# Kernel tuning notes

Hardware: AMD Instinct MI355X
Metric: run time of the kernel (lower is better)

The kernel has to match this reference:

```python
import jax, jax.numpy as jnp
import numpy as np

B, S = 16, 1024
D_MODEL, N_MEL = 256, 80
IN_DIM = D_MODEL * (((N_MEL - 1) // 2 - 1) // 2)  # 4864
G, V, CV_DIM = 2, 320, 256


def setup_inputs() -> dict:
    key = jax.random.key(0)
    k1, k2, k3 = jax.random.split(key, 3)
    hidden_states = jax.random.normal(k1, (B, S, IN_DIM), dtype=jnp.float32)
    W = jax.random.normal(k2, (IN_DIM, G * V), dtype=jnp.float32) / np.sqrt(IN_DIM)
    b = jnp.zeros((G * V,), dtype=jnp.float32)
    codevectors = jax.random.normal(k3, (1, G * V, CV_DIM // G), dtype=jnp.float32)
    return {"hidden_states": hidden_states, "W": W, "b": b,
            "codevectors": codevectors, "num_groups": G}


def reference(hidden_states, W, b, codevectors, num_groups):
    bsz, seq, _ = hidden_states.shape
    logits = hidden_states @ W + b                      # (B, S, G*V)
    gv = logits.shape[-1]
    nvars = gv // num_groups
    flat = logits.reshape(bsz * seq, num_groups, nvars)  # (BS, G, V)
    idx = jnp.argmax(flat, axis=-1)                      # (BS, G) int
    # one-hot codevector probs (eval / hard argmax branch)
    probs = jax.nn.one_hot(idx, nvars, dtype=logits.dtype)  # (BS, G, V)
    marginal = probs.mean(axis=0)                        # (G, V)
    perplexity = jnp.exp(-jnp.sum(marginal * jnp.log(marginal + 1e-7), axis=-1)).sum()
    # weighted sum over codebook == gather of selected codevector per group
    cv = codevectors.reshape(num_groups, nvars, -1)      # (G, V, Dg)
    gathered = cv[jnp.arange(num_groups)[None, :], idx]  # (BS, G, Dg)
    out = gathered.reshape(bsz, seq, -1)                 # (B, S, codevector_dim)
    return (out, perplexity)
```

## Files before the change

kernel.cpp:

```cpp
#include <hip/hip_runtime.h>
#include <stdint.h>

#define M_TOT 16384
#define K_TOT 4864
#define N_TOT 640
#define GRP   2
#define NV    320
#define CVD   128

#define BM 128
#define BN 320
#define BK 32
#define KITERS (K_TOT / BK)

#define MARGIN 2.0e-3f

typedef __attribute__((ext_vector_type(8))) short short8;
typedef __attribute__((ext_vector_type(4))) float f32x4;

#define WS_FLAGCNT  0
#define WS_COUNTS   256
#define WS_FLAGLIST 4096
#define WS_PACKED   (4096 + 262144)
#define WS_WT       (1u << 20)

__device__ __forceinline__ unsigned int mono_u32(float f) {
    unsigned int b = __float_as_uint(f);
    return b ^ ((unsigned int)((int)b >> 31) | 0x80000000u);
}
__device__ __forceinline__ unsigned short f2bf(float x) {
    unsigned int u = __float_as_uint(x);
    return (unsigned short)((u + 0x7fffu + ((u >> 16) & 1u)) >> 16);
}
__device__ __forceinline__ float bf2f(unsigned short h) {
    return __uint_as_float(((unsigned int)h) << 16);
}
__device__ __forceinline__ void gld16(const void* g, void* l) {
    __builtin_amdgcn_global_load_lds(
        (const __attribute__((address_space(1))) unsigned int*)g,
        (__attribute__((address_space(3))) unsigned int*)l, 16, 0, 0);
}

__global__ __launch_bounds__(256)
void convert_wt(const float* __restrict__ W, unsigned short* __restrict__ wt)
{
    __shared__ float sW[64][68];
    const int k0 = blockIdx.x * 64;
    const int n0 = blockIdx.y * 64;
    const int tid = threadIdx.x;
    for (int l = tid; l < 64 * 16; l += 256) {
        int kr = l >> 4, nc = (l & 15) * 4;
        float4 v = *(const float4*)(W + (size_t)(k0 + kr) * N_TOT + n0 + nc);
        sW[kr][nc] = v.x; sW[kr][nc + 1] = v.y; sW[kr][nc + 2] = v.z; sW[kr][nc + 3] = v.w;
    }
    __syncthreads();
    unsigned short* whi = wt;
    unsigned short* wlo = wt + (size_t)N_TOT * K_TOT;
    for (int l = tid; l < 64 * 8; l += 256) {
        int nr = l >> 3, ko = (l & 7) * 8;
        union { short8 v; unsigned short u[8]; } hu, lu;
#pragma unroll
        for (int j = 0; j < 8; ++j) {
            float x = sW[ko + j][nr];
            unsigned short hb = f2bf(x);
            hu.u[j] = hb;
            lu.u[j] = f2bf(x - bf2f(hb));
        }
        size_t off = (size_t)(n0 + nr) * K_TOT + k0 + ko;
        *(short8*)(whi + off) = hu.v;
        *(short8*)(wlo + off) = lu.v;
    }
}

__device__ __forceinline__ void stage_b(const unsigned short* __restrict__ wt,
                                        short* sBbuf, int bx, int kk, int tid)
{
#pragma unroll
    for (int r = 0; r < 5; ++r) {
        int c = r * 512 + tid;
        int half = (c >= 1280) ? 1 : 0;
        int cc = c - half * 1280;
        int row = cc >> 2, oct = cc & 3;
        const unsigned short* gp = wt + (size_t)half * N_TOT * K_TOT
            + (size_t)(bx * NV + row) * K_TOT + kk + ((oct ^ (row & 3)) << 3);
        gld16(gp, sBbuf + (size_t)c * 8);
    }
}

__global__ __launch_bounds__(512, 2)
void gemm_mfma(const float* __restrict__ A, const unsigned short* __restrict__ wt,
               const float* __restrict__ bias,
               unsigned long long* __restrict__ packed,
               unsigned int* __restrict__ flagcnt, unsigned int* __restrict__ flaglist)
{
    __shared__ short sA[2][2][BM][BK];
    __shared__ short sB[2][2][BN][BK];
    __shared__ uint4 sRed[BM][4];

    const int tid  = threadIdx.x;
    const int L    = tid & 63;
    const int w    = tid >> 6;
    const int quad = L >> 4;
    const int lrow = L & 15;
    const int wrow = w >> 2;
    const int wcol = w & 3;
    const int bx   = blockIdx.x;
    const int m0   = blockIdx.y * BM;
    const int octr = quad ^ (L & 3);

    const int arow = tid >> 2;
    const int aoct = tid & 3;
    const float* Ap = A + (size_t)(m0 + arow) * K_TOT + aoct * 8;
    const int aswz = ((aoct ^ (arow & 3)) << 3);

    f32x4 acc[4][5];
#pragma unroll
    for (int i = 0; i < 4; ++i)
#pragma unroll
        for (int j = 0; j < 5; ++j) acc[i][j] = (f32x4){0.f, 0.f, 0.f, 0.f};

    {
        stage_b(wt, &sB[0][0][0][0], bx, 0, tid);
        float4 a0 = *(const float4*)(Ap);
        float4 a1 = *(const float4*)(Ap + 4);
        union { short8 v; unsigned short u[8]; } hu, lu;
        float xs[8] = {a0.x, a0.y, a0.z, a0.w, a1.x, a1.y, a1.z, a1.w};
#pragma unroll
        for (int j = 0; j < 8; ++j) {
            unsigned short hb = f2bf(xs[j]);
            hu.u[j] = hb; lu.u[j] = f2bf(xs[j] - bf2f(hb));
        }
        *(short8*)&sA[0][0][arow][aswz] = hu.v;
        *(short8*)&sA[0][1][arow][aswz] = lu.v;
    }
    __syncthreads();

    int k0 = 0;
    for (int it = 0; it < KITERS; ++it) {
        const int buf = it & 1;
        const int kn  = k0 + BK;
        float4 a0, a1;
        const bool more = (it + 1 < KITERS);
        if (more) {
            stage_b(wt, &sB[buf ^ 1][0][0][0], bx, kn, tid);
            a0 = *(const float4*)(Ap + kn);
            a1 = *(const float4*)(Ap + kn + 4);
        }
        short8 ah[4], al[4];
#pragma unroll
        for (int fi = 0; fi < 4; ++fi) {
            int mloc = wrow * 64 + fi * 16 + lrow;
            ah[fi] = *(const short8*)&sA[buf][0][mloc][octr * 8];
            al[fi] = *(const short8*)&sA[buf][1][mloc][octr * 8];
        }
#pragma unroll
        for (int fj = 0; fj < 5; ++fj) {
            int nloc = wcol * 80 + fj * 16 + lrow;
            short8 bh = *(const short8*)&sB[buf][0][nloc][octr * 8];
            short8 bl = *(const short8*)&sB[buf][1][nloc][octr * 8];
#pragma unroll
            for (int fi = 0; fi < 4; ++fi) {
                acc[fi][fj] = __builtin_amdgcn_mfma_f32_16x16x32_bf16(ah[fi], bh, acc[fi][fj], 0, 0, 0);
                acc[fi][fj] = __builtin_amdgcn_mfma_f32_16x16x32_bf16(ah[fi], bl, acc[fi][fj], 0, 0, 0);
                acc[fi][fj] = __builtin_amdgcn_mfma_f32_16x16x32_bf16(al[fi], bh, acc[fi][fj], 0, 0, 0);
            }
        }
        if (more) {
            union { short8 v; unsigned short u[8]; } hu, lu;
            float xs[8] = {a0.x, a0.y, a0.z, a0.w, a1.x, a1.y, a1.z, a1.w};
#pragma unroll
            for (int j = 0; j < 8; ++j) {
                unsigned short hb = f2bf(xs[j]);
                hu.u[j] = hb; lu.u[j] = f2bf(xs[j] - bf2f(hb));
            }
            *(short8*)&sA[buf ^ 1][0][arow][aswz] = hu.v;
            *(short8*)&sA[buf ^ 1][1][arow][aswz] = lu.v;
        }
        __syncthreads();
        k0 = kn;
    }

    float bs[5];
#pragma unroll
    for (int fj = 0; fj < 5; ++fj)
        bs[fj] = bias[bx * NV + wcol * 80 + fj * 16 + lrow];

#pragma unroll
    for (int fi = 0; fi < 4; ++fi) {
#pragma unroll
        for (int r = 0; r < 4; ++r) {
            unsigned long long pv = 0; float v1 = 0.f, v2 = -3.4e38f;
#pragma unroll
            for (int fj = 0; fj < 5; ++fj) {
                float v = acc[fi][fj][r] + bs[fj];
                int cig = wcol * 80 + fj * 16 + lrow;
                unsigned long long p = ((unsigned long long)mono_u32(v) << 32)
                                     | (unsigned int)(NV - 1 - cig);
                if (fj == 0) { pv = p; v1 = v; }
                else if (p > pv) { v2 = v1; v1 = v; pv = p; }
                else { v2 = fmaxf(v2, v); }
            }
#pragma unroll
            for (int msk = 1; msk < 16; msk <<= 1) {
                unsigned long long opv = __shfl_xor(pv, msk);
                float ov1 = __shfl_xor(v1, msk);
                float ov2 = __shfl_xor(v2, msk);
                if (opv > pv) { v2 = fmaxf(v1, ov2); v1 = ov1; pv = opv; }
                else          { v2 = fmaxf(v2, ov1); }
            }
            if (lrow == 0) {
                int row_blk = wrow * 64 + fi * 16 + quad * 4 + r;
                uint4 e;
                e.x = (unsigned int)(pv & 0xFFFFFFFFull);
                e.y = (unsigned int)(pv >> 32);
                e.z = __float_as_uint(v2);
                e.w = __float_as_uint(v1);
                sRed[row_blk][wcol] = e;
            }
        }
    }
    __syncthreads();

    if (tid < BM) {
        unsigned long long pv = 0; float v1 = -3.4e38f, v2 = -3.4e38f;
#pragma unroll
        for (int wc = 0; wc < 4; ++wc) {
            uint4 e = sRed[tid][wc];
            unsigned long long opv = ((unsigned long long)e.y << 32) | e.x;
            float ov1 = __uint_as_float(e.w), ov2 = __uint_as_float(e.z);
            if (opv > pv) { v2 = fmaxf(v1, ov2); v1 = ov1; pv = opv; }
            else          { v2 = fmaxf(v2, ov1); }
        }
        packed[(size_t)(m0 + tid) * GRP + bx] = pv;
        if (v1 - v2 <= MARGIN) {
            unsigned int slot = atomicAdd(flagcnt, 1u);
            flaglist[slot] = ((unsigned int)(m0 + tid) << 1) | (unsigned int)bx;
        }
    }
}

__global__ __launch_bounds__(320)
void recheck(const float* __restrict__ A, const float* __restrict__ W,
             const float* __restrict__ bias,
             const unsigned int* __restrict__ flagcnt,
             const unsigned int* __restrict__ flaglist,
             unsigned long long* __restrict__ packed)
{
    __shared__ float  sAr[K_TOT];
    __shared__ float4 sPart[320];
    __shared__ float  sVals[NV];
    const int tid = threadIdx.x;
    const unsigned int cnt = *flagcnt;
    const int kseg = tid / 80, c4 = tid % 80;
    for (unsigned int i = blockIdx.x; i < cnt; i += gridDim.x) {
        unsigned int item = flaglist[i];
        int row = (int)(item >> 1), g = (int)(item & 1);
        __syncthreads();
        for (int l = tid; l < K_TOT / 4; l += 320)
            *(float4*)&sAr[l * 4] = *(const float4*)(A + (size_t)row * K_TOT + l * 4);
        __syncthreads();
        float4 acc = {0.f, 0.f, 0.f, 0.f};
        const float* wp = W + (size_t)(kseg * 1216) * N_TOT + g * NV + c4 * 4;
        const float* ap = sAr + kseg * 1216;
        for (int k = 0; k < 1216; ++k) {
            float a = ap[k];
            float4 wv = *(const float4*)(wp + (size_t)k * N_TOT);
            acc.x = fmaf(a, wv.x, acc.x);
            acc.y = fmaf(a, wv.y, acc.y);
            acc.z = fmaf(a, wv.z, acc.z);
            acc.w = fmaf(a, wv.w, acc.w);
        }
        sPart[tid] = acc;
        __syncthreads();
        if (tid < 80) {
            float4 s = {0.f, 0.f, 0.f, 0.f};
#pragma unroll
            for (int ks = 0; ks < 4; ++ks) {
                float4 p = sPart[ks * 80 + tid];
                s.x += p.x; s.y += p.y; s.z += p.z; s.w += p.w;
            }
            float4 bb = *(const float4*)(bias + g * NV + tid * 4);
            sVals[tid * 4 + 0] = s.x + bb.x;
            sVals[tid * 4 + 1] = s.y + bb.y;
            sVals[tid * 4 + 2] = s.z + bb.z;
            sVals[tid * 4 + 3] = s.w + bb.w;
        }
        __syncthreads();
        if (tid == 0) {
            float best = sVals[0]; int bi = 0;
            for (int c = 1; c < NV; ++c)
                if (sVals[c] > best) { best = sVals[c]; bi = c; }
            packed[(size_t)row * GRP + g] =
                ((unsigned long long)mono_u32(best) << 32) | (unsigned int)(NV - 1 - bi);
        }
    }
}

__global__ __launch_bounds__(256)
void gather_hist(const unsigned long long* __restrict__ packed,
                 const float* __restrict__ cv,
                 float* __restrict__ out, int* __restrict__ counts)
{
    const int m = blockIdx.x;
    const int t = threadIdx.x;
    const int g = t >> 7;
    const unsigned long long p = packed[(size_t)m * GRP + g];
    const int idx = (NV - 1) - (int)(p & 0xFFFFFFFFull);
    const int c = t & 127;
    out[(size_t)m * (GRP * CVD) + t] = cv[((size_t)g * NV + idx) * CVD + c];
    if (c == 0) atomicAdd(&counts[g * NV + idx], 1);
}

__global__ void perplexity_k(const int* __restrict__ counts, float* __restrict__ outp)
{
    __shared__ float sred[GRP * NV];
    const int t = threadIdx.x;
    const float marg = (float)counts[t] * (1.0f / (float)M_TOT);
    sred[t] = marg * logf(marg + 1e-7f);
    __syncthreads();
    if (t < GRP) {
        float s = 0.f;
        for (int i = 0; i < NV; ++i) s += sred[t * NV + i];
        sred[t] = expf(-s);
    }
    __syncthreads();
    if (t == 0) outp[0] = sred[0] + sred[1];
}

extern "C" void kernel_launch(void* const* d_in, const int* in_sizes, int n_in,
                              void* d_out, int out_size, void* d_ws, size_t ws_size,
                              hipStream_t stream)
{
    const float* A    = (const float*)d_in[0];
    const float* Wm   = (const float*)d_in[1];
    const float* bias = (const float*)d_in[2];
    const float* cv   = (const float*)d_in[3];

    float* out = (float*)d_out;
    float* ppl = out + (size_t)M_TOT * (GRP * CVD);

    char* ws = (char*)d_ws;
    unsigned int*       flagcnt  = (unsigned int*)(ws + WS_FLAGCNT);
    int*                counts   = (int*)(ws + WS_COUNTS);
    unsigned int*       flaglist = (unsigned int*)(ws + WS_FLAGLIST);
    unsigned long long* packed   = (unsigned long long*)(ws + WS_PACKED);
    unsigned short*     wt       = (unsigned short*)(ws + WS_WT);

    hipMemsetAsync(d_ws, 0, 4096, stream);
    convert_wt<<<dim3(76, 10), 256, 0, stream>>>(Wm, wt);
    gemm_mfma<<<dim3(2, 128), 512, 0, stream>>>(A, wt, bias, packed, flagcnt, flaglist);
    recheck<<<256, 320, 0, stream>>>(A, Wm, bias, flagcnt, flaglist, packed);
    gather_hist<<<M_TOT, 256, 0, stream>>>(packed, cv, out, counts);
    perplexity_k<<<1, GRP * NV, 0, stream>>>(counts, ppl);
}
```

Measured before the change: 808.2 us.

## Use 4-wave GEMM blocks with larger per-wave tiles and batch recheck rows

The GEMM goes from 8 waves per block to 4. Each wave now covers all 128 rows and an 80-column slice, so each B fragment read from shared memory is reused across 8 A fragments instead of 4. The hi/lo bf16 halves are interleaved into one 64-wide shared row with an XOR swizzle. The recheck kernel handles 4 flagged rows per block iteration, so the weight streaming loop serves several rows at once. The cost is fewer waves per CU (launch bounds 256,1) and higher register pressure from 160 accumulator floats per lane, which may hurt latency hiding.

```diff
diff --git a/kernel.cpp b/kernel.cpp
--- a/kernel.cpp
+++ b/kernel.cpp
@@ -76,25 +76,25 @@
                                         short* sBbuf, int bx, int kk, int tid)
 {
 #pragma unroll
-    for (int r = 0; r < 5; ++r) {
-        int c = r * 512 + tid;
-        int half = (c >= 1280) ? 1 : 0;
-        int cc = c - half * 1280;
-        int row = cc >> 2, oct = cc & 3;
+    for (int r = 0; r < 10; ++r) {
+        int c = r * 256 + tid;
+        int row = c >> 3, slot = c & 7;
+        int sv = slot ^ (row & 7);
+        int half = sv >> 2, oct = sv & 3;
         const unsigned short* gp = wt + (size_t)half * N_TOT * K_TOT
-            + (size_t)(bx * NV + row) * K_TOT + kk + ((oct ^ (row & 3)) << 3);
+            + (size_t)(bx * NV + row) * K_TOT + kk + (oct << 3);
         gld16(gp, sBbuf + (size_t)c * 8);
     }
 }
 
-__global__ __launch_bounds__(512, 2)
+__global__ __launch_bounds__(256, 1)
 void gemm_mfma(const float* __restrict__ A, const unsigned short* __restrict__ wt,
                const float* __restrict__ bias,
                unsigned long long* __restrict__ packed,
                unsigned int* __restrict__ flagcnt, unsigned int* __restrict__ flaglist)
 {
-    __shared__ short sA[2][2][BM][BK];
-    __shared__ short sB[2][2][BN][BK];
+    __shared__ short sA[2][BM][64];
+    __shared__ short sB[2][BN][64];
     __shared__ uint4 sRed[BM][4];
 
     const int tid  = threadIdx.x;
@@ -102,36 +102,47 @@
     const int w    = tid >> 6;
     const int quad = L >> 4;
     const int lrow = L & 15;
-    const int wrow = w >> 2;
-    const int wcol = w & 3;
     const int bx   = blockIdx.x;
     const int m0   = blockIdx.y * BM;
-    const int octr = quad ^ (L & 3);
-
-    const int arow = tid >> 2;
-    const int aoct = tid & 3;
-    const float* Ap = A + (size_t)(m0 + arow) * K_TOT + aoct * 8;
-    const int aswz = ((aoct ^ (arow & 3)) << 3);
-
-    f32x4 acc[4][5];
-#pragma unroll
-    for (int i = 0; i < 4; ++i)
+
+    const int sh = (quad ^ (lrow & 7)) << 3;
+    const int sl = ((4 | quad) ^ (lrow & 7)) << 3;
+
+    const int arow = tid >> 1;
+    const int apar = tid & 1;
+    const float* Ap = A + (size_t)(m0 + arow) * K_TOT + apar * 16;
+    const int o0 = 2 * apar, o1 = 2 * apar + 1;
+    const int sH0 = (o0 ^ (arow & 7)) << 3;
+    const int sH1 = (o1 ^ (arow & 7)) << 3;
+    const int sL0 = ((4 | o0) ^ (arow & 7)) << 3;
+    const int sL1 = ((4 | o1) ^ (arow & 7)) << 3;
+
+    f32x4 acc[8][5];
+#pragma unroll
+    for (int i = 0; i < 8; ++i)
 #pragma unroll
         for (int j = 0; j < 5; ++j) acc[i][j] = (f32x4){0.f, 0.f, 0.f, 0.f};
 
     {
-        stage_b(wt, &sB[0][0][0][0], bx, 0, tid);
+        stage_b(wt, &sB[0][0][0], bx, 0, tid);
         float4 a0 = *(const float4*)(Ap);
         float4 a1 = *(const float4*)(Ap + 4);
-        union { short8 v; unsigned short u[8]; } hu, lu;
-        float xs[8] = {a0.x, a0.y, a0.z, a0.w, a1.x, a1.y, a1.z, a1.w};
+        float4 a2 = *(const float4*)(Ap + 8);
+        float4 a3 = *(const float4*)(Ap + 12);
+        union { short8 v; unsigned short u[8]; } h0, l0, h1, l1;
+        float xs0[8] = {a0.x, a0.y, a0.z, a0.w, a1.x, a1.y, a1.z, a1.w};
+        float xs1[8] = {a2.x, a2.y, a2.z, a2.w, a3.x, a3.y, a3.z, a3.w};
 #pragma unroll
         for (int j = 0; j < 8; ++j) {
-            unsigned short hb = f2bf(xs[j]);
-            hu.u[j] = hb; lu.u[j] = f2bf(xs[j] - bf2f(hb));
-        }
-        *(short8*)&sA[0][0][arow][aswz] = hu.v;
-        *(short8*)&sA[0][1][arow][aswz] = lu.v;
+            unsigned short hb = f2bf(xs0[j]);
+            h0.u[j] = hb; l0.u[j] = f2bf(xs0[j] - bf2f(hb));
+            unsigned short hc = f2bf(xs1[j]);
+            h1.u[j] = hc; l1.u[j] = f2bf(xs1[j] - bf2f(hc));
+        }
+        *(short8*)&sA[0][arow][sH0] = h0.v;
+        *(short8*)&sA[0][arow][sH1] = h1.v;
+        *(short8*)&sA[0][arow][sL0] = l0.v;
+        *(short8*)&sA[0][arow][sL1] = l1.v;
     }
     __syncthreads();
 
@@ -139,42 +150,49 @@
     for (int it = 0; it < KITERS; ++it) {
         const int buf = it & 1;
         const int kn  = k0 + BK;
-        float4 a0, a1;
+        float4 a0, a1, a2, a3;
         const bool more = (it + 1 < KITERS);
         if (more) {
-            stage_b(wt, &sB[buf ^ 1][0][0][0], bx, kn, tid);
+            stage_b(wt, &sB[buf ^ 1][0][0], bx, kn, tid);
             a0 = *(const float4*)(Ap + kn);
             a1 = *(const float4*)(Ap + kn + 4);
-        }
-        short8 ah[4], al[4];
-#pragma unroll
-        for (int fi = 0; fi < 4; ++fi) {
-            int mloc = wrow * 64 + fi * 16 + lrow;
-            ah[fi] = *(const short8*)&sA[buf][0][mloc][octr * 8];
-            al[fi] = *(const short8*)&sA[buf][1][mloc][octr * 8];
+            a2 = *(const float4*)(Ap + kn + 8);
+            a3 = *(const float4*)(Ap + kn + 12);
+        }
+        short8 ah[8], al[8];
+#pragma unroll
+        for (int fi = 0; fi < 8; ++fi) {
+            int mloc = fi * 16 + lrow;
+            ah[fi] = *(const short8*)&sA[buf][mloc][sh];
+            al[fi] = *(const short8*)&sA[buf][mloc][sl];
         }
 #pragma unroll
         for (int fj = 0; fj < 5; ++fj) {
-            int nloc = wcol * 80 + fj * 16 + lrow;
-            short8 bh = *(const short8*)&sB[buf][0][nloc][octr * 8];
-            short8 bl = *(const short8*)&sB[buf][1][nloc][octr * 8];
-#pragma unroll
-            for (int fi = 0; fi < 4; ++fi) {
+            int nloc = w * 80 + fj * 16 + lrow;
+            short8 bh = *(const short8*)&sB[buf][nloc][sh];
+            short8 bl = *(const short8*)&sB[buf][nloc][sl];
+#pragma unroll
+            for (int fi = 0; fi < 8; ++fi) {
                 acc[fi][fj] = __builtin_amdgcn_mfma_f32_16x16x32_bf16(ah[fi], bh, acc[fi][fj], 0, 0, 0);
                 acc[fi][fj] = __builtin_amdgcn_mfma_f32_16x16x32_bf16(ah[fi], bl, acc[fi][fj], 0, 0, 0);
                 acc[fi][fj] = __builtin_amdgcn_mfma_f32_16x16x32_bf16(al[fi], bh, acc[fi][fj], 0, 0, 0);
             }
         }
         if (more) {
-            union { short8 v; unsigned short u[8]; } hu, lu;
-            float xs[8] = {a0.x, a0.y, a0.z, a0.w, a1.x, a1.y, a1.z, a1.w};
+            union { short8 v; unsigned short u[8]; } h0, l0, h1, l1;
+            float xs0[8] = {a0.x, a0.y, a0.z, a0.w, a1.x, a1.y, a1.z, a1.w};
+            float xs1[8] = {a2.x, a2.y, a2.z, a2.w, a3.x, a3.y, a3.z, a3.w};
 #pragma unroll
             for (int j = 0; j < 8; ++j) {
-                unsigned short hb = f2bf(xs[j]);
-                hu.u[j] = hb; lu.u[j] = f2bf(xs[j] - bf2f(hb));
-            }
-            *(short8*)&sA[buf ^ 1][0][arow][aswz] = hu.v;
-            *(short8*)&sA[buf ^ 1][1][arow][aswz] = lu.v;
+                unsigned short hb = f2bf(xs0[j]);
+                h0.u[j] = hb; l0.u[j] = f2bf(xs0[j] - bf2f(hb));
+                unsigned short hc = f2bf(xs1[j]);
+                h1.u[j] = hc; l1.u[j] = f2bf(xs1[j] - bf2f(hc));
+            }
+            *(short8*)&sA[buf ^ 1][arow][sH0] = h0.v;
+            *(short8*)&sA[buf ^ 1][arow][sH1] = h1.v;
+            *(short8*)&sA[buf ^ 1][arow][sL0] = l0.v;
+            *(short8*)&sA[buf ^ 1][arow][sL1] = l1.v;
         }
         __syncthreads();
         k0 = kn;
@@ -183,17 +201,17 @@
     float bs[5];
 #pragma unroll
     for (int fj = 0; fj < 5; ++fj)
-        bs[fj] = bias[bx * NV + wcol * 80 + fj * 16 + lrow];
-
-#pragma unroll
-    for (int fi = 0; fi < 4; ++fi) {
+        bs[fj] = bias[bx * NV + w * 80 + fj * 16 + lrow];
+
+#pragma unroll
+    for (int fi = 0; fi < 8; ++fi) {
 #pragma unroll
         for (int r = 0; r < 4; ++r) {
             unsigned long long pv = 0; float v1 = 0.f, v2 = -3.4e38f;
 #pragma unroll
             for (int fj = 0; fj < 5; ++fj) {
                 float v = acc[fi][fj][r] + bs[fj];
-                int cig = wcol * 80 + fj * 16 + lrow;
+                int cig = w * 80 + fj * 16 + lrow;
                 unsigned long long p = ((unsigned long long)mono_u32(v) << 32)
                                      | (unsigned int)(NV - 1 - cig);
                 if (fj == 0) { pv = p; v1 = v; }
@@ -209,13 +227,13 @@
                 else          { v2 = fmaxf(v2, ov1); }
             }
             if (lrow == 0) {
-                int row_blk = wrow * 64 + fi * 16 + quad * 4 + r;
+                int row_blk = fi * 16 + quad * 4 + r;
                 uint4 e;
                 e.x = (unsigned int)(pv & 0xFFFFFFFFull);
                 e.y = (unsigned int)(pv >> 32);
                 e.z = __float_as_uint(v2);
                 e.w = __float_as_uint(v1);
-                sRed[row_blk][wcol] = e;
+                sRed[row_blk][w] = e;
             }
         }
     }
@@ -239,6 +257,7 @@
     }
 }
 
+#define RCH_IPB 4
 __global__ __launch_bounds__(320)
 void recheck(const float* __restrict__ A, const float* __restrict__ W,
              const float* __restrict__ bias,
@@ -246,51 +265,83 @@
              const unsigned int* __restrict__ flaglist,
              unsigned long long* __restrict__ packed)
 {
-    __shared__ float  sAr[K_TOT];
-    __shared__ float4 sPart[320];
-    __shared__ float  sVals[NV];
+    __shared__ float  sAr[RCH_IPB][K_TOT];
+    __shared__ float4 sPart[RCH_IPB][320];
+    __shared__ float  sVals[RCH_IPB][NV];
+    __shared__ int    sRow[RCH_IPB], sG[RCH_IPB];
     const int tid = threadIdx.x;
     const unsigned int cnt = *flagcnt;
     const int kseg = tid / 80, c4 = tid % 80;
-    for (unsigned int i = blockIdx.x; i < cnt; i += gridDim.x) {
-        unsigned int item = flaglist[i];
-        int row = (int)(item >> 1), g = (int)(item & 1);
-        __syncthreads();
-        for (int l = tid; l < K_TOT / 4; l += 320)
-            *(float4*)&sAr[l * 4] = *(const float4*)(A + (size_t)row * K_TOT + l * 4);
-        __syncthreads();
-        float4 acc = {0.f, 0.f, 0.f, 0.f};
-        const float* wp = W + (size_t)(kseg * 1216) * N_TOT + g * NV + c4 * 4;
-        const float* ap = sAr + kseg * 1216;
+    for (unsigned int base = (unsigned int)blockIdx.x * RCH_IPB; base < cnt;
+         base += (unsigned int)gridDim.x * RCH_IPB) {
+        const unsigned int nit = (cnt - base < (unsigned int)RCH_IPB)
+                               ? (cnt - base) : (unsigned int)RCH_IPB;
+        __syncthreads();
+        if (tid < RCH_IPB) {
+            unsigned int src = base + (unsigned int)tid;
+            if (src >= cnt) src = base;
+            unsigned int item = flaglist[src];
+            sRow[tid] = (int)(item >> 1);
+            sG[tid]   = (int)(item & 1);
+        }
+        __syncthreads();
+        for (int l = tid; l < RCH_IPB * (K_TOT / 4); l += 320) {
+            int j = l / (K_TOT / 4), off = l - j * (K_TOT / 4);
+            *(float4*)&sAr[j][off * 4] =
+                *(const float4*)(A + (size_t)sRow[j] * K_TOT + off * 4);
+        }
+        __syncthreads();
+        float4 ac0 = {0.f,0.f,0.f,0.f}, ac1 = {0.f,0.f,0.f,0.f};
+        float4 ac2 = {0.f,0.f,0.f,0.f}, ac3 = {0.f,0.f,0.f,0.f};
+        const float* wbase = W + (size_t)(kseg * 1216) * N_TOT + c4 * 4;
+        const float* w0 = wbase + sG[0] * NV;
+        const float* w1 = wbase + sG[1] * NV;
+        const float* w2 = wbase + sG[2] * NV;
+        const float* w3 = wbase + sG[3] * NV;
+        const float* a0p = &sAr[0][kseg * 1216];
+        const float* a1p = &sAr[1][kseg * 1216];
+        const float* a2p = &sAr[2][kseg * 1216];
+        const float* a3p = &sAr[3][kseg * 1216];
         for (int k = 0; k < 1216; ++k) {
-            float a = ap[k];
-            float4 wv = *(const float4*)(wp + (size_t)k * N_TOT);
-            acc.x = fmaf(a, wv.x, acc.x);
-            acc.y = fmaf(a, wv.y, acc.y);
-            acc.z = fmaf(a, wv.z, acc.z);
-            acc.w = fmaf(a, wv.w, acc.w);
-        }
-        sPart[tid] = acc;
+            size_t ro = (size_t)k * N_TOT;
+            float4 wv0 = *(const float4*)(w0 + ro); float av0 = a0p[k];
+            ac0.x = fmaf(av0, wv0.x, ac0.x); ac0.y = fmaf(av0, wv0.y, ac0.y);
+            ac0.z = fmaf(av0, wv0.z, ac0.z); ac0.w = fmaf(av0, wv0.w, ac0.w);
+            float4 wv1 = *(const float4*)(w1 + ro); float av1 = a1p[k];
+            ac1.x = fmaf(av1, wv1.x, ac1.x); ac1.y = fmaf(av1, wv1.y, ac1.y);
+            ac1.z = fmaf(av1, wv1.z, ac1.z); ac1.w = fmaf(av1, wv1.w, ac1.w);
+            float4 wv2 = *(const float4*)(w2 + ro); float av2 = a2p[k];
+            ac2.x = fmaf(av2, wv2.x, ac2.x); ac2.y = fmaf(av2, wv2.y, ac2.y);
+            ac2.z = fmaf(av2, wv2.z, ac2.z); ac2.w = fmaf(av2, wv2.w, ac2.w);
+            float4 wv3 = *(const float4*)(w3 + ro); float av3 = a3p[k];
+            ac3.x = fmaf(av3, wv3.x, ac3.x); ac3.y = fmaf(av3, wv3.y, ac3.y);
+            ac3.z = fmaf(av3, wv3.z, ac3.z); ac3.w = fmaf(av3, wv3.w, ac3.w);
+        }
+        sPart[0][tid] = ac0; sPart[1][tid] = ac1;
+        sPart[2][tid] = ac2; sPart[3][tid] = ac3;
         __syncthreads();
         if (tid < 80) {
-            float4 s = {0.f, 0.f, 0.f, 0.f};
-#pragma unroll
-            for (int ks = 0; ks < 4; ++ks) {
-                float4 p = sPart[ks * 80 + tid];
-                s.x += p.x; s.y += p.y; s.z += p.z; s.w += p.w;
-            }
-            float4 bb = *(const float4*)(bias + g * NV + tid * 4);
-            sVals[tid * 4 + 0] = s.x + bb.x;
-            sVals[tid * 4 + 1] = s.y + bb.y;
-            sVals[tid * 4 + 2] = s.z + bb.z;
-            sVals[tid * 4 + 3] = s.w + bb.w;
-        }
-        __syncthreads();
-        if (tid == 0) {
-            float best = sVals[0]; int bi = 0;
+#pragma unroll
+            for (int j = 0; j < RCH_IPB; ++j) {
+                float4 s = {0.f, 0.f, 0.f, 0.f};
+#pragma unroll
+                for (int ks = 0; ks < 4; ++ks) {
+                    float4 p = sPart[j][ks * 80 + tid];
+                    s.x += p.x; s.y += p.y; s.z += p.z; s.w += p.w;
+                }
+                float4 bb = *(const float4*)(bias + sG[j] * NV + tid * 4);
+                sVals[j][tid * 4 + 0] = s.x + bb.x;
+                sVals[j][tid * 4 + 1] = s.y + bb.y;
+                sVals[j][tid * 4 + 2] = s.z + bb.z;
+                sVals[j][tid * 4 + 3] = s.w + bb.w;
+            }
+        }
+        __syncthreads();
+        if (tid < (int)nit) {
+            float best = sVals[tid][0]; int bi = 0;
             for (int c = 1; c < NV; ++c)
-                if (sVals[c] > best) { best = sVals[c]; bi = c; }
-            packed[(size_t)row * GRP + g] =
+                if (sVals[tid][c] > best) { best = sVals[tid][c]; bi = c; }
+            packed[(size_t)sRow[tid] * GRP + sG[tid]] =
                 ((unsigned long long)mono_u32(best) << 32) | (unsigned int)(NV - 1 - bi);
         }
     }
@@ -348,7 +399,7 @@
 
     hipMemsetAsync(d_ws, 0, 4096, stream);
     convert_wt<<<dim3(76, 10), 256, 0, stream>>>(Wm, wt);
-    gemm_mfma<<<dim3(2, 128), 512, 0, stream>>>(A, wt, bias, packed, flagcnt, flaglist);
+    gemm_mfma<<<dim3(2, 128), 256, 0, stream>>>(A, wt, bias, packed, flagcnt, flaglist);
     recheck<<<256, 320, 0, stream>>>(A, Wm, bias, flagcnt, flaglist, packed);
     gather_hist<<<M_TOT, 256, 0, stream>>>(packed, cv, out, counts);
     perplexity_k<<<1, GRP * NV, 0, stream>>>(counts, ppl);
```

New measurement: 1.042 ms. 1.29x slower.
